# Optimization experiments

Measured on AMD Instinct MI355X. Metric: run time of the kernel, lower is better.

The kernel has to match this reference:

```python
import jax, jax.numpy as jnp
import numpy as np

D_MODEL = 2048
EXPAND = 2
D_INNER = EXPAND * D_MODEL          # 4096 == d_ssm
D_STATE = 128
NGROUPS = 1
HEADDIM = 64
NHEADS = D_INNER // HEADDIM          # 64
D_CONV = 4
CHUNK = 128
D_XBC = D_INNER + 2 * NGROUPS * D_STATE   # 4352
D_IN_PROJ = 2 * D_INNER + 2 * NGROUPS * D_STATE + NHEADS  # 8512
EPS = 1e-5


def setup_inputs() -> dict:
    key = jax.random.key(0)
    ks = jax.random.split(key, 9)
    u = jax.random.normal(ks[0], (2, 2048, D_MODEL), dtype=jnp.float32)
    W_in = jax.random.normal(ks[1], (D_IN_PROJ, D_MODEL), dtype=jnp.float32) / np.sqrt(D_MODEL)
    conv_w = jax.random.normal(ks[2], (D_XBC, D_CONV), dtype=jnp.float32) / np.sqrt(D_CONV)
    conv_b = jax.random.normal(ks[3], (D_XBC,), dtype=jnp.float32) * 0.1
    dt_bias = jnp.log(jnp.expm1(jax.random.uniform(ks[4], (NHEADS,), minval=0.001, maxval=0.1)))
    A_log = jnp.log(jax.random.uniform(ks[5], (NHEADS,), minval=1.0, maxval=16.0))
    D = jnp.ones((NHEADS,), dtype=jnp.float32)
    norm_weight = jnp.ones((D_INNER,), dtype=jnp.float32)
    W_out = jax.random.normal(ks[8], (D_MODEL, D_INNER), dtype=jnp.float32) / np.sqrt(D_INNER)
    return {"u": u, "W_in": W_in, "conv_w": conv_w, "conv_b": conv_b,
            "dt_bias": dt_bias, "A_log": A_log, "D": D,
            "norm_weight": norm_weight, "W_out": W_out}


def _causal_conv1d(xBC, conv_w, conv_b):
    # xBC: [b, l, d]; depthwise causal conv of width D_CONV, then SiLU
    x = jnp.transpose(xBC, (0, 2, 1))                      # [b, d, l]
    x = jnp.pad(x, ((0, 0), (0, 0), (D_CONV - 1, 0)))
    y = jax.lax.conv_general_dilated(
        x, conv_w[:, None, :], window_strides=(1,), padding='VALID',
        feature_group_count=D_XBC, dimension_numbers=('NCH', 'OIH', 'NCH'))
    y = y + conv_b[None, :, None]
    return jnp.transpose(jax.nn.silu(y), (0, 2, 1))        # [b, l, d]


def _ssd(x, dt, A, B, C, D):
    # x: [b,l,h,p]; dt: [b,l,h] (post-softplus); A: [h]; B,C: [b,l,g,n]; D: [h]
    b, L, h, p = x.shape
    n = B.shape[-1]
    c = L // CHUNK
    hpg = h // NGROUPS
    Bh = jnp.repeat(B, hpg, axis=2)                        # [b,l,h,n]
    Ch = jnp.repeat(C, hpg, axis=2)
    xr = x.reshape(b, c, CHUNK, h, p)
    dtr = dt.reshape(b, c, CHUNK, h)
    Br = Bh.reshape(b, c, CHUNK, h, n)
    Cr = Ch.reshape(b, c, CHUNK, h, n)
    xdt = xr * dtr[..., None]                              # [b,c,l,h,p]
    dA = jnp.transpose((dt * A[None, None, :]).reshape(b, c, CHUNK, h), (0, 3, 1, 2))  # [b,h,c,l]
    A_cs = jnp.cumsum(dA, axis=-1)                         # [b,h,c,l]
    # intra-chunk decay matrix L[i,j] = exp(sum_{j+1..i} dA), lower-triangular
    diff = A_cs[..., :, None] - A_cs[..., None, :]         # [b,h,c,l,s]
    mask = jnp.tril(jnp.ones((CHUNK, CHUNK), dtype=bool))
    Lmat = jnp.where(mask, jnp.exp(jnp.where(mask, diff, 0.0)), 0.0)
    Y_diag = jnp.einsum('bclhn,bcshn,bhcls,bcshp->bclhp', Cr, Br, Lmat, xdt)
    decay_states = jnp.exp(A_cs[..., -1:] - A_cs)          # [b,h,c,l]
    states = jnp.einsum('bclhn,bhcl,bclhp->bchpn', Br, decay_states, xdt)
    chunk_decay = jnp.exp(A_cs[..., -1])                   # [b,h,c]
    # inter-chunk recurrence over c chunks
    def step(carry, inp):
        s, d = inp                                         # s:[b,h,p,n], d:[b,h]
        return carry * d[..., None, None] + s, carry
    init = jnp.zeros((b, h, p, n), dtype=x.dtype)
    _, prev = jax.lax.scan(step, init,
                           (jnp.transpose(states, (1, 0, 2, 3, 4)),
                            jnp.transpose(chunk_decay, (2, 0, 1))))
    prev_states = jnp.transpose(prev, (1, 0, 2, 3, 4))     # [b,c,h,p,n]
    Y_off = jnp.einsum('bclhn,bchpn,bhcl->bclhp', Cr, prev_states, jnp.exp(A_cs))
    Y = (Y_diag + Y_off).reshape(b, L, h, p) + x * D[None, None, :, None]
    return Y


def reference(u, W_in, conv_w, conv_b, dt_bias, A_log, D, norm_weight, W_out):
    b, L, _ = u.shape
    zxbcdt = jnp.einsum('bld,ed->ble', u, W_in)            # [b,l,8512]
    z = zxbcdt[..., :D_INNER]
    xBC = zxbcdt[..., D_INNER:D_INNER + D_XBC]
    dt = zxbcdt[..., D_INNER + D_XBC:]                     # [b,l,h]
    xBC = _causal_conv1d(xBC, conv_w, conv_b)
    x = xBC[..., :D_INNER]
    B = xBC[..., D_INNER:D_INNER + NGROUPS * D_STATE].reshape(b, L, NGROUPS, D_STATE)
    C = xBC[..., D_INNER + NGROUPS * D_STATE:].reshape(b, L, NGROUPS, D_STATE)
    dt = jax.nn.softplus(dt + dt_bias[None, None, :])
    A = -jnp.exp(A_log)
    y = _ssd(x.reshape(b, L, NHEADS, HEADDIM), dt, A, B, C, D)
    y = y.reshape(b, L, D_INNER)
    # gated RMSNorm (norm_before_gate=False): norm(y * silu(z))
    yg = y * jax.nn.silu(z)
    y = yg * jax.lax.rsqrt(jnp.mean(yg * yg, axis=-1, keepdims=True) + EPS) * norm_weight
    return jnp.einsum('bld,ed->ble', y, W_out)
```

## Files before the change

kernel.cpp:

```cpp
#include <hip/hip_runtime.h>
#include <cstdint>
#include <cstddef>

#define SEQ     2048
#define NBATCH  2
#define BL      (NBATCH*SEQ)
#define DMODEL  2048
#define DINNER  4096
#define DSTATE  128
#define HEADDIM 64
#define NHEADS  64
#define DXBC    4352
#define DPROJ   8512
#define NPAD    8704
#define NCHUNK  16
#define CHUNKL  128

typedef __bf16 bf16x8_t __attribute__((ext_vector_type(8)));
typedef float f32x4_t __attribute__((ext_vector_type(4)));
typedef unsigned short u16x8_t __attribute__((ext_vector_type(8)));
typedef unsigned short u16x4_t __attribute__((ext_vector_type(4)));
typedef __attribute__((address_space(1))) unsigned int as1_u32;
typedef __attribute__((address_space(3))) unsigned int as3_u32;

__device__ __forceinline__ unsigned short f2bf(float f) {
  unsigned u = __builtin_bit_cast(unsigned, f);
  u += 0x7FFFu + ((u >> 16) & 1u);
  return (unsigned short)(u >> 16);
}
__device__ __forceinline__ float bf2f(unsigned short h) {
  unsigned u = ((unsigned)h) << 16;
  return __builtin_bit_cast(float, u);
}
__device__ __forceinline__ void gload16(const void* g, void* l) {
  __builtin_amdgcn_global_load_lds((const as1_u32*)g, (as3_u32*)l, 16, 0, 0);
}
__device__ __forceinline__ f32x4_t mfma16(u16x8_t a, u16x8_t b, f32x4_t c) {
  return __builtin_amdgcn_mfma_f32_16x16x32_bf16(
      __builtin_bit_cast(bf16x8_t, a), __builtin_bit_cast(bf16x8_t, b), c, 0, 0, 0);
}
__device__ __forceinline__ float siluf(float x) { return x / (1.f + __expf(-x)); }

#define GB_U   (BL * DMODEL / 4 / 256)
#define GB_WIN (NPAD * DMODEL / 4 / 256)
__global__ __launch_bounds__(256) void cvt_uw_kernel(const float* __restrict__ u,
                                                     unsigned short* __restrict__ u_bf,
                                                     const float* __restrict__ W_in,
                                                     unsigned short* __restrict__ win_bf) {
  int blk = blockIdx.x;
  if (blk < GB_U) {
    int idx = (blk * 256 + threadIdx.x) * 4;
    float4 v = *(const float4*)&u[idx];
    u16x4_t o; o[0] = f2bf(v.x); o[1] = f2bf(v.y); o[2] = f2bf(v.z); o[3] = f2bf(v.w);
    *(u16x4_t*)&u_bf[idx] = o;
  } else {
    int idx = ((blk - GB_U) * 256 + threadIdx.x) * 4;
    int e = idx / DMODEL;
    u16x4_t o;
    if (e < DPROJ) {
      float4 v = *(const float4*)&W_in[idx];
      o[0] = f2bf(v.x); o[1] = f2bf(v.y); o[2] = f2bf(v.z); o[3] = f2bf(v.w);
    } else {
      o[0] = 0; o[1] = 0; o[2] = 0; o[3] = 0;
    }
    *(u16x4_t*)&win_bf[idx] = o;
  }
}

template <int WM, bool BF16OUT>
__global__ __launch_bounds__(512, 2) void gemm256_kernel(const unsigned short* __restrict__ A,
                                                         const unsigned short* __restrict__ B,
                                                         void* __restrict__ Cp,
                                                         int M, int N, int K, int gx) {
  constexpr int BM  = 32 * WM;
  constexpr int AUB = BM * 64;
  constexpr int BUB = 16384;
  constexpr int BUF = AUB + BUB;
  constexpr int LA  = AUB / 8192;
  constexpr int LB  = 2;
  constexpr int LT  = LA + LB;
  __shared__ __attribute__((aligned(16))) char lds[4 * BUF];

  const int nwg = gridDim.x;
  const int q8 = nwg >> 3;
  const int lid = blockIdx.x;
  const int newid = (lid & 7) * q8 + (lid >> 3);
  const int band = newid / (gx * 4);
  const int idx  = newid % (gx * 4);
  const int n0 = (idx >> 2) * 256;
  const int m0 = (band * 4 + (idx & 3)) * BM;

  const int t = threadIdx.x, lane = t & 63, w = t >> 6;
  const int wm = w >> 2, wn = w & 3;
  const int NK = K >> 5;
  const int kslot = (lane >> 4) * 16;

  f32x4_t acc[WM][4];
#pragma unroll
  for (int i = 0; i < WM; ++i)
#pragma unroll
    for (int j = 0; j < 4; ++j) acc[i][j] = (f32x4_t){0.f, 0.f, 0.f, 0.f};

  auto stage_unit = [&](int u) {
    if (u >= 2 * NK) return;
    const int Tt = u >> 1;
    char* base = lds + (Tt & 3) * BUF + ((u & 1) ? AUB : 0);
    const unsigned short* G = (u & 1) ? B : A;
    const int g0 = (u & 1) ? n0 : m0;
    const int k0 = Tt << 5;
    if (u & 1) {
#pragma unroll
      for (int i = 0; i < LB; ++i) {
        int o = i * 8192 + t * 16;
        int row = o >> 6;
        int cb = (o & 63) ^ (((row >> 1) & 3) << 4);
        gload16(&G[(size_t)(g0 + row) * K + k0 + (cb >> 1)], base + o);
      }
    } else {
#pragma unroll
      for (int i = 0; i < LA; ++i) {
        int o = i * 8192 + t * 16;
        int row = o >> 6;
        int cb = (o & 63) ^ (((row >> 1) & 3) << 4);
        gload16(&G[(size_t)(g0 + row) * K + k0 + (cb >> 1)], base + o);
      }
    }
  };
  auto rdA = [&](int bq, int mr) -> u16x8_t {
    int row = wm * (BM / 2) + mr * 16 + (lane & 15);
    int byte = bq * BUF + row * 64 + (kslot ^ (((row >> 1) & 3) << 4));
    return *(const u16x8_t*)(lds + byte);
  };
  auto rdB = [&](int bq, int nr) -> u16x8_t {
    int row = wn * 64 + nr * 16 + (lane & 15);
    int byte = bq * BUF + AUB + row * 64 + (kslot ^ (((row >> 1) & 3) << 4));
    return *(const u16x8_t*)(lds + byte);
  };

#pragma unroll
  for (int u = 0; u < 6; ++u) stage_unit(u);

  for (int T = 0; T < NK; ++T) {
    const int bq = T & 3;
    if (T <= NK - 3)      { if constexpr (LT == 4) asm volatile("s_waitcnt vmcnt(8)" ::: "memory");
                            else                   asm volatile("s_waitcnt vmcnt(6)" ::: "memory"); }
    else if (T == NK - 2) { if constexpr (LT == 4) asm volatile("s_waitcnt vmcnt(4)" ::: "memory");
                            else                   asm volatile("s_waitcnt vmcnt(3)" ::: "memory"); }
    else                  asm volatile("s_waitcnt vmcnt(0)" ::: "memory");
    __builtin_amdgcn_s_barrier();
    asm volatile("" ::: "memory");
    __builtin_amdgcn_sched_barrier(0);

    u16x8_t af[WM], bfr[4];
#pragma unroll
    for (int mr = 0; mr < WM; ++mr) af[mr] = rdA(bq, mr);
    bfr[0] = rdB(bq, 0);
    bfr[1] = rdB(bq, 1);
    stage_unit(2 * T + 6);
    __builtin_amdgcn_s_setprio(1);
#pragma unroll
    for (int mr = 0; mr < WM; ++mr) {
      acc[mr][0] = mfma16(af[mr], bfr[0], acc[mr][0]);
      acc[mr][1] = mfma16(af[mr], bfr[1], acc[mr][1]);
    }
    __builtin_amdgcn_s_setprio(0);
    bfr[2] = rdB(bq, 2);
    bfr[3] = rdB(bq, 3);
    stage_unit(2 * T + 7);
    __builtin_amdgcn_s_setprio(1);
#pragma unroll
    for (int mr = 0; mr < WM; ++mr) {
      acc[mr][2] = mfma16(af[mr], bfr[2], acc[mr][2]);
      acc[mr][3] = mfma16(af[mr], bfr[3], acc[mr][3]);
    }
    __builtin_amdgcn_s_setprio(0);
  }

#pragma unroll
  for (int mr = 0; mr < WM; ++mr) {
    const int mbase = m0 + wm * (BM / 2) + mr * 16 + (lane >> 4) * 4;
#pragma unroll
    for (int nr = 0; nr < 4; ++nr) {
      const int n = n0 + wn * 64 + nr * 16 + (lane & 15);
#pragma unroll
      for (int r = 0; r < 4; ++r) {
        if (BF16OUT) ((unsigned short*)Cp)[(size_t)(mbase + r) * N + n] = f2bf(acc[mr][nr][r]);
        else         ((float*)Cp)[(size_t)(mbase + r) * N + n] = acc[mr][nr][r];
      }
    }
  }
}

#define GB_WOUT (DMODEL * DINNER / 4 / 256)
#define GB_CONV (BL * (DXBC / 8) / 256)
#define GB_DT   (NBATCH * NHEADS * NCHUNK / 2)
__global__ __launch_bounds__(256) void postg1_kernel(const float* __restrict__ W_out,
                                                     unsigned short* __restrict__ wout_bf,
                                                     const unsigned short* __restrict__ zx,
                                                     const float* __restrict__ conv_w,
                                                     const float* __restrict__ conv_b,
                                                     unsigned short* __restrict__ xc,
                                                     const float* __restrict__ dt_bias,
                                                     const float* __restrict__ A_log,
                                                     float* __restrict__ dt_soft,
                                                     float* __restrict__ Acs,
                                                     float* __restrict__ cdecay) {
  __shared__ float sbuf[256];
  int blk = blockIdx.x;
  int t = threadIdx.x;
  if (blk < GB_WOUT) {
    int idx = (blk * 256 + t) * 4;
    float4 v = *(const float4*)&W_out[idx];
    u16x4_t o; o[0] = f2bf(v.x); o[1] = f2bf(v.y); o[2] = f2bf(v.z); o[3] = f2bf(v.w);
    *(u16x4_t*)&wout_bf[idx] = o;
  } else if (blk < GB_WOUT + GB_CONV) {
    int idx = (blk - GB_WOUT) * 256 + t;
    int e8 = (idx % (DXBC / 8)) * 8;
    int bl = idx / (DXBC / 8);
    int l = bl % SEQ, b = bl / SEQ;
    float acc[8];
#pragma unroll
    for (int j = 0; j < 8; ++j) acc[j] = conv_b[e8 + j];
    const unsigned short* zrow = zx + (size_t)b * SEQ * NPAD + DINNER + e8;
#pragma unroll
    for (int wi = 0; wi < 4; ++wi) {
      int ll = l - 3 + wi;
      if (ll >= 0) {
        u16x8_t v = *(const u16x8_t*)(zrow + (size_t)ll * NPAD);
#pragma unroll
        for (int j = 0; j < 8; ++j) acc[j] += bf2f(v[j]) * conv_w[(e8 + j) * 4 + wi];
      }
    }
    u16x8_t o;
#pragma unroll
    for (int j = 0; j < 8; ++j) o[j] = f2bf(siluf(acc[j]));
    *(u16x8_t*)(xc + (size_t)bl * DXBC + e8) = o;
  } else {
    int id = (blk - GB_WOUT - GB_CONV) * 2 + (t >> 7);
    int i = t & 127;
    int c = id & 15, h = (id >> 4) & 63, b = id >> 10;
    int l = c * CHUNKL + i;
    float raw = bf2f(zx[((size_t)b * SEQ + l) * NPAD + (DINNER + DXBC) + h]) + dt_bias[h];
    float dt = (raw > 20.f) ? raw : log1pf(__expf(raw));
    dt_soft[((size_t)b * 64 + h) * SEQ + l] = dt;
    float A = -__expf(A_log[h]);
    float* sb = sbuf + (t >> 7) * 128;
    sb[i] = dt * A;
    __syncthreads();
    for (int ofs = 1; ofs < 128; ofs <<= 1) {
      float v = (i >= ofs) ? sb[i - ofs] : 0.f;
      __syncthreads();
      sb[i] += v;
      __syncthreads();
    }
    float cs = sb[i];
    Acs[(((size_t)b * 64 + h) * 16 + c) * 128 + i] = cs;
    if (i == 127) cdecay[((size_t)b * 64 + h) * 16 + c] = __expf(cs);
  }
}

#define GB_XDT (NBATCH * NHEADS * NCHUNK)
__global__ __launch_bounds__(256) void xdtbtr_kernel(const unsigned short* __restrict__ xc,
                                                     const float* __restrict__ dt_soft,
                                                     unsigned short* __restrict__ xdtT,
                                                     unsigned short* __restrict__ BT) {
  __shared__ __attribute__((aligned(16))) char smem[33536];
  int blk = blockIdx.x;
  int t = threadIdx.x;
  if (blk < GB_XDT) {
    int lt = blk & 15, h = (blk >> 4) & 63, b = blk >> 10;
    unsigned short (*tile)[66] = (unsigned short(*)[66])smem;
    float* dts = (float*)(smem + 16896);
    const unsigned short* xg = xc + ((size_t)b * SEQ + lt * 128) * DXBC + h * 64;
#pragma unroll
    for (int k = 0; k < 32; ++k) {
      int idx = t + k * 256;
      int row = idx >> 6, col = idx & 63;
      tile[row][col] = xg[(size_t)row * DXBC + col];
    }
    if (t < 128) dts[t] = dt_soft[((size_t)b * 64 + h) * SEQ + lt * 128 + t];
    __syncthreads();
    unsigned short* xo = xdtT + (((size_t)b * 64 + h) * 64) * SEQ + lt * 128;
#pragma unroll
    for (int k = 0; k < 32; ++k) {
      int idx = t + k * 256;
      int p = idx >> 7, j = idx & 127;
      xo[(size_t)p * SEQ + j] = f2bf(bf2f(tile[j][p]) * dts[j]);
    }
  } else {
    int bb = blk - GB_XDT;
    int lt = bb & 15, b = bb >> 4;
    unsigned short (*tile)[129] = (unsigned short(*)[129])smem;
    const unsigned short* src = xc + ((size_t)b * SEQ + lt * 128) * DXBC + DINNER;
#pragma unroll
    for (int k = 0; k < 64; ++k) {
      int idx = t + k * 256;
      int j = idx >> 7, n = idx & 127;
      tile[j][n] = src[(size_t)j * DXBC + n];
    }
    __syncthreads();
    unsigned short* dst = BT + (size_t)b * 128 * SEQ + lt * 128;
#pragma unroll
    for (int k = 0; k < 64; ++k) {
      int idx = t + k * 256;
      int n = idx >> 7, j = idx & 127;
      dst[(size_t)n * SEQ + j] = tile[j][n];
    }
  }
}

__global__ __launch_bounds__(256) void ssd_states_kernel(const unsigned short* __restrict__ BT,
                                                         const unsigned short* __restrict__ xdtT,
                                                         const float* __restrict__ Acs,
                                                         unsigned short* __restrict__ states) {
  int blk = blockIdx.x;
  int h = blk & 63, c = (blk >> 6) & 15, b = blk >> 10;
  __shared__ unsigned short BTs[128 * 128];
  __shared__ unsigned short xs[64 * 128];
  __shared__ float dec[128];
  int t = threadIdx.x, lane = t & 63, w = t >> 6, wr = w >> 1, wc = w & 1;
  int srow = t >> 4, scol = (t & 15) * 8;
  const unsigned short* BTb = BT + (size_t)b * 128 * SEQ + c * 128;
#pragma unroll
  for (int s = 0; s < 8; ++s) {
    int r = s * 16 + srow;
    gload16(&BTb[(size_t)r * SEQ + scol], &BTs[r * 128 + scol]);
  }
  const unsigned short* xb = xdtT + (((size_t)b * 64 + h) * 64) * SEQ + c * 128;
#pragma unroll
  for (int s = 0; s < 4; ++s) {
    int r = s * 16 + srow;
    gload16(&xb[(size_t)r * SEQ + scol], &xs[r * 128 + scol]);
  }
  const float* acsr = Acs + (((size_t)b * 64 + h) * 16 + c) * 128;
  float alast = acsr[127];
  if (t < 128) dec[t] = __expf(alast - acsr[t]);
  __syncthreads();

  f32x4_t acc[2][4];
#pragma unroll
  for (int i = 0; i < 2; ++i)
#pragma unroll
    for (int j = 0; j < 4; ++j) acc[i][j] = (f32x4_t){0.f, 0.f, 0.f, 0.f};
#pragma unroll
  for (int ks = 0; ks < 4; ++ks) {
    const int kk = ks * 32 + (lane >> 4) * 8;
    float d8[8];
#pragma unroll
    for (int e = 0; e < 8; ++e) d8[e] = dec[kk + e];
    u16x8_t af[2], bfr[4];
#pragma unroll
    for (int i = 0; i < 2; ++i) {
      u16x8_t raw = *(const u16x8_t*)&xs[(wr * 32 + i * 16 + (lane & 15)) * 128 + kk];
      u16x8_t sc;
#pragma unroll
      for (int e = 0; e < 8; ++e) sc[e] = f2bf(bf2f(raw[e]) * d8[e]);
      af[i] = sc;
    }
#pragma unroll
    for (int j = 0; j < 4; ++j)
      bfr[j] = *(const u16x8_t*)&BTs[(wc * 64 + j * 16 + (lane & 15)) * 128 + kk];
#pragma unroll
    for (int i = 0; i < 2; ++i)
#pragma unroll
      for (int j = 0; j < 4; ++j) acc[i][j] = mfma16(af[i], bfr[j], acc[i][j]);
  }
  unsigned short* so = states + ((((size_t)b * 16 + c) * 64 + h) * 64) * 128;
#pragma unroll
  for (int i = 0; i < 2; ++i) {
    int pbase = wr * 32 + i * 16 + (lane >> 4) * 4;
#pragma unroll
    for (int j = 0; j < 4; ++j) {
      int n = wc * 64 + j * 16 + (lane & 15);
#pragma unroll
      for (int r = 0; r < 4; ++r) so[(size_t)(pbase + r) * 128 + n] = f2bf(acc[i][j][r]);
    }
  }
}

__global__ __launch_bounds__(256) void ssd_scan_kernel(const unsigned short* __restrict__ states,
                                                       const float* __restrict__ cdecay,
                                                       unsigned short* __restrict__ prevb) {
  int blk = blockIdx.x;
  int s = blk & 7, h = (blk >> 3) & 63, b = blk >> 9;
  int t = threadIdx.x;
  const size_t eoff = (size_t)s * 1024 + t * 4;
  const float* cd = cdecay + ((size_t)b * 64 + h) * 16;
  u16x4_t vals[16];
#pragma unroll
  for (int c = 0; c < 16; ++c) {
    const unsigned short* sp = states + (((size_t)(b * 16 + c) * 64 + h) * 64) * 128 + eoff;
    vals[c] = *(const u16x4_t*)sp;
  }
  float carry[4] = {0.f, 0.f, 0.f, 0.f};
#pragma unroll
  for (int c = 0; c < 16; ++c) {
    unsigned short* pp = prevb + (((size_t)(b * 16 + c) * 64 + h) * 64) * 128 + eoff;
    u16x4_t o;
#pragma unroll
    for (int k = 0; k < 4; ++k) o[k] = f2bf(carry[k]);
    *(u16x4_t*)pp = o;
    float d = cd[c];
#pragma unroll
    for (int k = 0; k < 4; ++k) carry[k] = carry[k] * d + bf2f(vals[c][k]);
  }
}

__global__ __launch_bounds__(256) void ssd_y_kernel(const unsigned short* __restrict__ xc,
                                                    const unsigned short* __restrict__ xdtT,
                                                    const unsigned short* __restrict__ prevb,
                                                    const float* __restrict__ Acs,
                                                    const float* __restrict__ Dp,
                                                    unsigned short* __restrict__ Y) {
  int blk = blockIdx.x;
  int h = blk & 63, c = (blk >> 6) & 15, b = blk >> 10;
  __shared__ unsigned short Bs[128 * 128];
  __shared__ unsigned short Cs[128 * 128];
  __shared__ unsigned short xs[64 * 128];
  int t = threadIdx.x, lane = t & 63, w = t >> 6, wr = w >> 1, wc = w & 1;
  int srow = t >> 4, scol = (t & 15) * 8;
  const unsigned short* Bg = xc + ((size_t)b * SEQ + c * 128) * DXBC + DINNER;
  const unsigned short* Cg = Bg + DSTATE;
#pragma unroll
  for (int s = 0; s < 8; ++s) {
    int r = s * 16 + srow;
    gload16(&Bg[(size_t)r * DXBC + scol], &Bs[r * 128 + scol]);
    gload16(&Cg[(size_t)r * DXBC + scol], &Cs[r * 128 + scol]);
  }
  const unsigned short* xg = xdtT + (((size_t)b * 64 + h) * 64) * SEQ + c * 128;
#pragma unroll
  for (int s = 0; s < 4; ++s) {
    int r = s * 16 + srow;
    gload16(&xg[(size_t)r * SEQ + scol], &xs[r * 128 + scol]);
  }
  const unsigned short* pg = prevb + ((((size_t)b * 16 + c) * 64 + h) * 64) * 128;
  u16x8_t pf_all[4][2];
#pragma unroll
  for (int ks = 0; ks < 4; ++ks) {
    const int kk = ks * 32 + (lane >> 4) * 8;
#pragma unroll
    for (int j = 0; j < 2; ++j)
      pf_all[ks][j] = *(const u16x8_t*)&pg[(size_t)(wc * 32 + j * 16 + (lane & 15)) * 128 + kk];
  }
  const float* acsr = Acs + (((size_t)b * 64 + h) * 16 + c) * 128;
  __syncthreads();

  f32x4_t cbt[4][4];
#pragma unroll
  for (int i = 0; i < 4; ++i)
#pragma unroll
    for (int j = 0; j < 4; ++j) cbt[i][j] = (f32x4_t){0.f, 0.f, 0.f, 0.f};
#pragma unroll
  for (int ks = 0; ks < 4; ++ks) {
    const int kk = ks * 32 + (lane >> 4) * 8;
    u16x8_t af[4], bfr[4];
#pragma unroll
    for (int i = 0; i < 4; ++i) {
      af[i]  = *(const u16x8_t*)&Bs[(wr * 64 + i * 16 + (lane & 15)) * 128 + kk];
      bfr[i] = *(const u16x8_t*)&Cs[(wc * 64 + i * 16 + (lane & 15)) * 128 + kk];
    }
#pragma unroll
    for (int i = 0; i < 4; ++i)
#pragma unroll
      for (int j = 0; j < 4; ++j) cbt[i][j] = mfma16(af[i], bfr[j], cbt[i][j]);
  }
  __syncthreads();
#pragma unroll
  for (int fi = 0; fi < 4; ++fi) {
#pragma unroll
    for (int fj = 0; fj < 4; ++fj) {
      int i = wc * 64 + fj * 16 + (lane & 15);
      int jb = wr * 64 + fi * 16 + (lane >> 4) * 4;
      float ai = acsr[i];
      u16x4_t m4;
#pragma unroll
      for (int r = 0; r < 4; ++r) {
        int j = jb + r;
        float v = (i >= j) ? cbt[fi][fj][r] * __expf(ai - acsr[j]) : 0.f;
        m4[r] = f2bf(v);
      }
      *(u16x4_t*)&Bs[i * 128 + jb] = m4;
    }
  }
  __syncthreads();

  f32x4_t accY[4][2], accO[4][2];
#pragma unroll
  for (int i = 0; i < 4; ++i)
#pragma unroll
    for (int j = 0; j < 2; ++j) {
      accY[i][j] = (f32x4_t){0.f, 0.f, 0.f, 0.f};
      accO[i][j] = (f32x4_t){0.f, 0.f, 0.f, 0.f};
    }
#pragma unroll
  for (int ks = 0; ks < 4; ++ks) {
    const int kk = ks * 32 + (lane >> 4) * 8;
    u16x8_t af[4], bfr[2], cf[4];
#pragma unroll
    for (int i = 0; i < 4; ++i) {
      af[i] = *(const u16x8_t*)&Bs[(wr * 64 + i * 16 + (lane & 15)) * 128 + kk];
      cf[i] = *(const u16x8_t*)&Cs[(wr * 64 + i * 16 + (lane & 15)) * 128 + kk];
    }
#pragma unroll
    for (int j = 0; j < 2; ++j)
      bfr[j] = *(const u16x8_t*)&xs[(wc * 32 + j * 16 + (lane & 15)) * 128 + kk];
#pragma unroll
    for (int i = 0; i < 4; ++i)
#pragma unroll
      for (int j = 0; j < 2; ++j) {
        accY[i][j] = mfma16(af[i], bfr[j], accY[i][j]);
        accO[i][j] = mfma16(cf[i], pf_all[ks][j], accO[i][j]);
      }
  }
  float Dh = Dp[h];
  unsigned short* Yo = Y + ((size_t)b * SEQ + c * 128) * DINNER + h * 64;
  const unsigned short* xo = xc + ((size_t)b * SEQ + c * 128) * DXBC + h * 64;
#pragma unroll
  for (int fi = 0; fi < 4; ++fi) {
    int ibase = wr * 64 + fi * 16 + (lane >> 4) * 4;
#pragma unroll
    for (int r = 0; r < 4; ++r) {
      int i = ibase + r;
      float esc = __expf(acsr[i]);
#pragma unroll
      for (int fj = 0; fj < 2; ++fj) {
        int p = wc * 32 + fj * 16 + (lane & 15);
        float v = accY[fi][fj][r] + accO[fi][fj][r] * esc + bf2f(xo[(size_t)i * DXBC + p]) * Dh;
        Yo[(size_t)i * DINNER + p] = f2bf(v);
      }
    }
  }
}

__global__ __launch_bounds__(256) void norm_kernel(const unsigned short* __restrict__ Y,
                                                   const unsigned short* __restrict__ zx,
                                                   const float* __restrict__ nw,
                                                   unsigned short* __restrict__ yn) {
  int bl = blockIdx.x;
  const unsigned short* yr = Y + (size_t)bl * DINNER;
  const unsigned short* zr = zx + (size_t)bl * NPAD;
  int t = threadIdx.x;
  int base = t * 16;
  u16x8_t y0 = *(const u16x8_t*)&yr[base], y1 = *(const u16x8_t*)&yr[base + 8];
  u16x8_t z0 = *(const u16x8_t*)&zr[base], z1 = *(const u16x8_t*)&zr[base + 8];
  float vals[16];
  float ss = 0.f;
#pragma unroll
  for (int k = 0; k < 8; ++k) {
    float g = bf2f(y0[k]) * siluf(bf2f(z0[k]));
    vals[k] = g; ss += g * g;
  }
#pragma unroll
  for (int k = 0; k < 8; ++k) {
    float g = bf2f(y1[k]) * siluf(bf2f(z1[k]));
    vals[8 + k] = g; ss += g * g;
  }
#pragma unroll
  for (int o = 32; o > 0; o >>= 1) ss += __shfl_down(ss, o, 64);
  __shared__ float red[4];
  if ((t & 63) == 0) red[t >> 6] = ss;
  __syncthreads();
  float tot = red[0] + red[1] + red[2] + red[3];
  float rs = rsqrtf(tot * (1.f / (float)DINNER) + 1e-5f);
  u16x8_t o0, o1;
#pragma unroll
  for (int k = 0; k < 8; ++k) {
    o0[k] = f2bf(vals[k] * rs * nw[base + k]);
    o1[k] = f2bf(vals[8 + k] * rs * nw[base + 8 + k]);
  }
  *(u16x8_t*)&yn[(size_t)bl * DINNER + base] = o0;
  *(u16x8_t*)&yn[(size_t)bl * DINNER + base + 8] = o1;
}

extern "C" void kernel_launch(void* const* d_in, const int* in_sizes, int n_in,
                              void* d_out, int out_size, void* d_ws, size_t ws_size,
                              hipStream_t stream) {
  const float* u       = (const float*)d_in[0];
  const float* W_in    = (const float*)d_in[1];
  const float* conv_w  = (const float*)d_in[2];
  const float* conv_b  = (const float*)d_in[3];
  const float* dt_bias = (const float*)d_in[4];
  const float* A_log   = (const float*)d_in[5];
  const float* Dv      = (const float*)d_in[6];
  const float* norm_w  = (const float*)d_in[7];
  const float* W_out   = (const float*)d_in[8];
  float* out = (float*)d_out;
  (void)in_sizes; (void)n_in; (void)out_size;

  const size_t SZ_UBF    = (size_t)BL * DMODEL * 2;
  const size_t SZ_WIN    = (size_t)NPAD * DMODEL * 2;
  const size_t SZ_XDTT   = (size_t)NBATCH * NHEADS * HEADDIM * SEQ * 2;
  const size_t SZ_ZX     = (size_t)BL * NPAD * 2;
  const size_t SZ_XC     = (size_t)BL * DXBC * 2;
  const size_t SZ_BT     = (size_t)NBATCH * DSTATE * SEQ * 2;
  const size_t SZ_DTS    = (size_t)NBATCH * NHEADS * SEQ * 4;
  const size_t SZ_ACS    = (size_t)NBATCH * NHEADS * NCHUNK * 128 * 4;
  const size_t SZ_CDEC   = (size_t)NBATCH * NHEADS * NCHUNK * 4;
  const size_t SZ_STATES = (size_t)NBATCH * NCHUNK * NHEADS * HEADDIM * DSTATE * 2;
  const size_t SZ_PREV   = (size_t)NBATCH * NCHUNK * NHEADS * HEADDIM * DSTATE * 2;
  const size_t REGION_A  = SZ_UBF + SZ_WIN;

  char* ws = (char*)d_ws;
  size_t off = 0;
  auto alloc = [&](size_t bytes) { char* p = ws + off; off += (bytes + 255) & ~(size_t)255; return p; };

  char* regionA = alloc(REGION_A);
  unsigned short* zx     = (unsigned short*)alloc(SZ_ZX);
  unsigned short* xc     = (unsigned short*)alloc(SZ_XC);
  unsigned short* BT     = (unsigned short*)alloc(SZ_BT);
  float* dt_soft         = (float*)alloc(SZ_DTS);
  float* Acs             = (float*)alloc(SZ_ACS);
  float* cdecay          = (float*)alloc(SZ_CDEC);
  char* statesYb         = alloc(SZ_STATES);
  char* prevYn           = alloc(SZ_PREV);
  if (off > ws_size) return;

  unsigned short* u_bf    = (unsigned short*)regionA;
  unsigned short* win_bf  = (unsigned short*)(regionA + SZ_UBF);
  unsigned short* xdtT    = (unsigned short*)regionA;
  unsigned short* wout_bf = (unsigned short*)(regionA + SZ_XDTT);
  unsigned short* states  = (unsigned short*)statesYb;
  unsigned short* Yb      = (unsigned short*)statesYb;
  unsigned short* prevb   = (unsigned short*)prevYn;
  unsigned short* yn      = (unsigned short*)prevYn;

  cvt_uw_kernel<<<dim3(GB_U + GB_WIN), dim3(256), 0, stream>>>(u, u_bf, W_in, win_bf);

  gemm256_kernel<8, true><<<dim3((NPAD / 256) * (BL / 256)), dim3(512), 0, stream>>>(
      u_bf, win_bf, zx, BL, NPAD, DMODEL, NPAD / 256);

  postg1_kernel<<<dim3(GB_WOUT + GB_CONV + GB_DT), dim3(256), 0, stream>>>(
      W_out, wout_bf, zx, conv_w, conv_b, xc, dt_bias, A_log, dt_soft, Acs, cdecay);

  xdtbtr_kernel<<<dim3(GB_XDT + NBATCH * (SEQ / 128)), dim3(256), 0, stream>>>(
      xc, dt_soft, xdtT, BT);

  ssd_states_kernel<<<dim3(NBATCH * NCHUNK * NHEADS), dim3(256), 0, stream>>>(BT, xdtT, Acs, states);
  ssd_scan_kernel<<<dim3(NBATCH * NHEADS * 8), dim3(256), 0, stream>>>(states, cdecay, prevb);
  ssd_y_kernel<<<dim3(NBATCH * NCHUNK * NHEADS), dim3(256), 0, stream>>>(xc, xdtT, prevb, Acs, Dv, Yb);

  norm_kernel<<<dim3(BL), dim3(256), 0, stream>>>(Yb, zx, norm_w, yn);

  gemm256_kernel<4, false><<<dim3((DMODEL / 256) * (BL / 128)), dim3(512), 0, stream>>>(
      yn, wout_bf, out, BL, DMODEL, DINNER, DMODEL / 256);
}
```

Before: 545.2 us.

## Replace input-projection GEMM with 8-phase ping-pong pipelined 256x256 kernel

Adds a new GEMM kernel for the input projection with a 256x256 tile and 128KB of double-buffered LDS, which limits it to one block per CU. The K loop is split into eight phases that interleave half-tile global loads with MFMA work, using barriers, setprio and explicit vmcnt waits. It also remaps block IDs across 8 groups, presumably for XCD-aware L2 locality. The goal is to hide global-load latency better than the previous gemm256 kernel, at the cost of lower occupancy and more barriers.

```diff
diff --git a/kernel.cpp b/kernel.cpp
--- a/kernel.cpp
+++ b/kernel.cpp
@@ -64,6 +64,141 @@
       o[0] = 0; o[1] = 0; o[2] = 0; o[3] = 0;
     }
     *(u16x4_t*)&win_bf[idx] = o;
+  }
+}
+
+template <bool BF16OUT>
+__global__ __launch_bounds__(512, 1) void gemm8p_kernel(const unsigned short* __restrict__ A,
+                                                        const unsigned short* __restrict__ B,
+                                                        void* __restrict__ Cp,
+                                                        int M, int N, int K, int gx) {
+  __shared__ __attribute__((aligned(16))) char lds[131072];
+  const int nwg = gridDim.x;
+  const int q8 = nwg >> 3;
+  const int lid = blockIdx.x;
+  const int newid = (lid & 7) * q8 + (lid >> 3);
+  const int band = newid / (gx * 4);
+  const int idx  = newid % (gx * 4);
+  const int n0 = (idx >> 2) * 256;
+  const int m0 = (band * 4 + (idx & 3)) * 256;
+  const int t = threadIdx.x, lane = t & 63, w = t >> 6;
+  const int wm = w >> 2, wn = w & 3;
+  const int NK = K >> 6;
+  const int NT = NK >> 1;
+
+  f32x4_t acc[8][4];
+#pragma unroll
+  for (int i = 0; i < 8; ++i)
+#pragma unroll
+    for (int j = 0; j < 4; ++j) acc[i][j] = (f32x4_t){0.f, 0.f, 0.f, 0.f};
+
+  auto stage_half = [&](int tile, int half) {
+    if (tile >= NK) return;
+    const bool isB = half >= 2;
+    const int hh = half & 1;
+    const unsigned short* G = isB ? B : A;
+    const int g0 = (isB ? n0 : m0) + hh * 128;
+    const int k0 = tile << 6;
+    char* base = lds + (tile & 1) * 65536 + (isB ? 32768 : 0) + hh * 16384;
+#pragma unroll
+    for (int i = 0; i < 2; ++i) {
+      int o = i * 8192 + t * 16;
+      int row = o >> 7;
+      int sl  = (o >> 4) & 7;
+      gload16(&G[(size_t)(g0 + row) * K + k0 + ((sl ^ (row & 7)) << 3)], base + o);
+    }
+  };
+  auto rdA = [&](int buf, int mr, int kk) -> u16x8_t {
+    int row = wm * 128 + mr * 16 + (lane & 15);
+    int sl = kk * 4 + (lane >> 4);
+    int byte = buf * 65536 + row * 128 + (((sl ^ (row & 7))) << 4);
+    return *(const u16x8_t*)(lds + byte);
+  };
+  auto rdB = [&](int buf, int nr, int kk) -> u16x8_t {
+    int row = wn * 64 + nr * 16 + (lane & 15);
+    int sl = kk * 4 + (lane >> 4);
+    int byte = buf * 65536 + 32768 + row * 128 + (((sl ^ (row & 7))) << 4);
+    return *(const u16x8_t*)(lds + byte);
+  };
+
+  u16x8_t af[4][2], bf[4][2];
+
+#define PH_SYNC() do { __builtin_amdgcn_s_barrier(); \
+    asm volatile("s_waitcnt lgkmcnt(0)" ::: "memory"); \
+    __builtin_amdgcn_sched_barrier(0); } while (0)
+#define PH_END() __builtin_amdgcn_s_barrier()
+
+  auto mm = [&](int mrBase, int nrBase) {
+    __builtin_amdgcn_s_setprio(1);
+#pragma unroll
+    for (int m = 0; m < 4; ++m)
+#pragma unroll
+      for (int n = 0; n < 2; ++n) {
+        acc[mrBase + m][nrBase + n] = mfma16(af[m][0], bf[nrBase + n][0], acc[mrBase + m][nrBase + n]);
+        acc[mrBase + m][nrBase + n] = mfma16(af[m][1], bf[nrBase + n][1], acc[mrBase + m][nrBase + n]);
+      }
+    __builtin_amdgcn_s_setprio(0);
+  };
+
+  stage_half(0, 0); stage_half(0, 1); stage_half(0, 2); stage_half(0, 3);
+  stage_half(1, 2); stage_half(1, 3);
+  asm volatile("s_waitcnt vmcnt(4)" ::: "memory");
+  __builtin_amdgcn_s_barrier();
+
+  for (int j = 0; j < NT; ++j) {
+    const bool last = (j == NT - 1);
+    const int t1 = 2 * j + 1;
+#pragma unroll
+    for (int m = 0; m < 4; ++m) { af[m][0] = rdA(0, m, 0); af[m][1] = rdA(0, m, 1); }
+#pragma unroll
+    for (int n = 0; n < 2; ++n) { bf[n][0] = rdB(0, n, 0); bf[n][1] = rdB(0, n, 1); }
+    stage_half(t1, 0);
+    PH_SYNC(); mm(0, 0); PH_END();
+    bf[2][0] = rdB(0, 2, 0); bf[2][1] = rdB(0, 2, 1);
+    bf[3][0] = rdB(0, 3, 0); bf[3][1] = rdB(0, 3, 1);
+    stage_half(t1, 1);
+    PH_SYNC(); mm(0, 2); PH_END();
+#pragma unroll
+    for (int m = 0; m < 4; ++m) { af[m][0] = rdA(0, 4 + m, 0); af[m][1] = rdA(0, 4 + m, 1); }
+    stage_half(2 * j + 2, 2);
+    PH_SYNC(); mm(4, 0); PH_END();
+    stage_half(2 * j + 2, 3);
+    if (!last) asm volatile("s_waitcnt vmcnt(4)" ::: "memory");
+    else       asm volatile("s_waitcnt vmcnt(0)" ::: "memory");
+    PH_SYNC(); mm(4, 2); PH_END();
+#pragma unroll
+    for (int m = 0; m < 4; ++m) { af[m][0] = rdA(1, m, 0); af[m][1] = rdA(1, m, 1); }
+#pragma unroll
+    for (int n = 0; n < 2; ++n) { bf[n][0] = rdB(1, n, 0); bf[n][1] = rdB(1, n, 1); }
+    stage_half(2 * j + 2, 0);
+    PH_SYNC(); mm(0, 0); PH_END();
+    bf[2][0] = rdB(1, 2, 0); bf[2][1] = rdB(1, 2, 1);
+    bf[3][0] = rdB(1, 3, 0); bf[3][1] = rdB(1, 3, 1);
+    stage_half(2 * j + 2, 1);
+    PH_SYNC(); mm(0, 2); PH_END();
+#pragma unroll
+    for (int m = 0; m < 4; ++m) { af[m][0] = rdA(1, 4 + m, 0); af[m][1] = rdA(1, 4 + m, 1); }
+    stage_half(2 * j + 3, 2);
+    PH_SYNC(); mm(4, 0); PH_END();
+    stage_half(2 * j + 3, 3);
+    if (!last) asm volatile("s_waitcnt vmcnt(4)" ::: "memory");
+    PH_SYNC(); mm(4, 2); PH_END();
+  }
+#undef PH_SYNC
+#undef PH_END
+
+#pragma unroll
+  for (int mr = 0; mr < 8; ++mr) {
+    const int mbase = m0 + wm * 128 + mr * 16 + (lane >> 4) * 4;
+#pragma unroll
+    for (int nr = 0; nr < 4; ++nr) {
+      const int n = n0 + wn * 64 + nr * 16 + (lane & 15);
+#pragma unroll
+      for (int r = 0; r < 4; ++r) {
+        if (BF16OUT) ((unsigned short*)Cp)[(size_t)(mbase + r) * N + n] = f2bf(acc[mr][nr][r]);
+        else         ((float*)Cp)[(size_t)(mbase + r) * N + n] = acc[mr][nr][r];
+      }
+    }
   }
 }
 
@@ -626,7 +761,7 @@
 
   cvt_uw_kernel<<<dim3(GB_U + GB_WIN), dim3(256), 0, stream>>>(u, u_bf, W_in, win_bf);
 
-  gemm256_kernel<8, true><<<dim3((NPAD / 256) * (BL / 256)), dim3(512), 0, stream>>>(
+  gemm8p_kernel<true><<<dim3((NPAD / 256) * (BL / 256)), dim3(512), 0, stream>>>(
       u_bf, win_bf, zx, BL, NPAD, DMODEL, NPAD / 256);
 
   postg1_kernel<<<dim3(GB_WOUT + GB_CONV + GB_DT), dim3(256), 0, stream>>>(
```

After: 554.1 us. No clear change (+1.6%).

## Precompute per-chunk C·Bᵀ once and share it across heads in ssd_y

Applied to the files above, without the earlier changes.

With NGROUPS=1 every head of a chunk multiplies the same B and C, so the C·Bᵀ product was recomputed 64 times per chunk. Extra blocks in the transpose kernel now compute this 128x128 product once per (batch, chunk) and store it in fp32 global memory. ssd_y_kernel reads it back instead of loading B into LDS and running the MFMA loop, which drops the B load and one barrier. The cost is 4 MB of extra workspace and fp32 global reads per block; only 32 blocks do the shared product, reading B and C directly from global memory without LDS staging.

```diff
diff --git a/kernel.cpp b/kernel.cpp
--- a/kernel.cpp
+++ b/kernel.cpp
@@ -260,10 +260,12 @@
 }
 
 #define GB_XDT (NBATCH * NHEADS * NCHUNK)
+#define GB_BTR (NBATCH * (SEQ / 128))
 __global__ __launch_bounds__(256) void xdtbtr_kernel(const unsigned short* __restrict__ xc,
                                                      const float* __restrict__ dt_soft,
                                                      unsigned short* __restrict__ xdtT,
-                                                     unsigned short* __restrict__ BT) {
+                                                     unsigned short* __restrict__ BT,
+                                                     float* __restrict__ cbtG) {
   __shared__ __attribute__((aligned(16))) char smem[33536];
   int blk = blockIdx.x;
   int t = threadIdx.x;
@@ -287,7 +289,7 @@
       int p = idx >> 7, j = idx & 127;
       xo[(size_t)p * SEQ + j] = f2bf(bf2f(tile[j][p]) * dts[j]);
     }
-  } else {
+  } else if (blk < GB_XDT + GB_BTR) {
     int bb = blk - GB_XDT;
     int lt = bb & 15, b = bb >> 4;
     unsigned short (*tile)[129] = (unsigned short(*)[129])smem;
@@ -305,6 +307,42 @@
       int idx = t + k * 256;
       int n = idx >> 7, j = idx & 127;
       dst[(size_t)n * SEQ + j] = tile[j][n];
+    }
+  } else {
+    int id = blk - GB_XDT - GB_BTR;
+    int c = id & 15, b = id >> 4;
+    int lane = t & 63, w4 = t >> 6;
+    int wr = w4 >> 1, wc = w4 & 1;
+    const unsigned short* Bg = xc + ((size_t)b * SEQ + c * 128) * DXBC + DINNER;
+    const unsigned short* Cg = Bg + DSTATE;
+    f32x4_t cbt[4][4];
+#pragma unroll
+    for (int i = 0; i < 4; ++i)
+#pragma unroll
+      for (int j = 0; j < 4; ++j) cbt[i][j] = (f32x4_t){0.f, 0.f, 0.f, 0.f};
+#pragma unroll
+    for (int ks = 0; ks < 4; ++ks) {
+      const int kk = ks * 32 + (lane >> 4) * 8;
+      u16x8_t af[4], bfr[4];
+#pragma unroll
+      for (int i = 0; i < 4; ++i) {
+        af[i]  = *(const u16x8_t*)&Bg[(size_t)(wr * 64 + i * 16 + (lane & 15)) * DXBC + kk];
+        bfr[i] = *(const u16x8_t*)&Cg[(size_t)(wc * 64 + i * 16 + (lane & 15)) * DXBC + kk];
+      }
+#pragma unroll
+      for (int i = 0; i < 4; ++i)
+#pragma unroll
+        for (int j = 0; j < 4; ++j) cbt[i][j] = mfma16(af[i], bfr[j], cbt[i][j]);
+    }
+    float* dst = cbtG + ((size_t)(b * 16 + c) * 128) * 128;
+#pragma unroll
+    for (int fi = 0; fi < 4; ++fi) {
+#pragma unroll
+      for (int fj = 0; fj < 4; ++fj) {
+        int i = wc * 64 + fj * 16 + (lane & 15);
+        int jb = wr * 64 + fi * 16 + (lane >> 4) * 4;
+        *(f32x4_t*)&dst[(size_t)i * 128 + jb] = cbt[fi][fj];
+      }
     }
   }
 }
@@ -410,21 +448,20 @@
                                                     const unsigned short* __restrict__ xdtT,
                                                     const unsigned short* __restrict__ prevb,
                                                     const float* __restrict__ Acs,
+                                                    const float* __restrict__ cbtG,
                                                     const float* __restrict__ Dp,
                                                     unsigned short* __restrict__ Y) {
   int blk = blockIdx.x;
   int h = blk & 63, c = (blk >> 6) & 15, b = blk >> 10;
-  __shared__ unsigned short Bs[128 * 128];
+  __shared__ unsigned short Ms[128 * 128];
   __shared__ unsigned short Cs[128 * 128];
   __shared__ unsigned short xs[64 * 128];
   int t = threadIdx.x, lane = t & 63, w = t >> 6, wr = w >> 1, wc = w & 1;
   int srow = t >> 4, scol = (t & 15) * 8;
-  const unsigned short* Bg = xc + ((size_t)b * SEQ + c * 128) * DXBC + DINNER;
-  const unsigned short* Cg = Bg + DSTATE;
+  const unsigned short* Cg = xc + ((size_t)b * SEQ + c * 128) * DXBC + DINNER + DSTATE;
 #pragma unroll
   for (int s = 0; s < 8; ++s) {
     int r = s * 16 + srow;
-    gload16(&Bg[(size_t)r * DXBC + scol], &Bs[r * 128 + scol]);
     gload16(&Cg[(size_t)r * DXBC + scol], &Cs[r * 128 + scol]);
   }
   const unsigned short* xg = xdtT + (((size_t)b * 64 + h) * 64) * SEQ + c * 128;
@@ -443,43 +480,23 @@
       pf_all[ks][j] = *(const u16x8_t*)&pg[(size_t)(wc * 32 + j * 16 + (lane & 15)) * 128 + kk];
   }
   const float* acsr = Acs + (((size_t)b * 64 + h) * 16 + c) * 128;
-  __syncthreads();
-
-  f32x4_t cbt[4][4];
-#pragma unroll
-  for (int i = 0; i < 4; ++i)
-#pragma unroll
-    for (int j = 0; j < 4; ++j) cbt[i][j] = (f32x4_t){0.f, 0.f, 0.f, 0.f};
-#pragma unroll
-  for (int ks = 0; ks < 4; ++ks) {
-    const int kk = ks * 32 + (lane >> 4) * 8;
-    u16x8_t af[4], bfr[4];
-#pragma unroll
-    for (int i = 0; i < 4; ++i) {
-      af[i]  = *(const u16x8_t*)&Bs[(wr * 64 + i * 16 + (lane & 15)) * 128 + kk];
-      bfr[i] = *(const u16x8_t*)&Cs[(wc * 64 + i * 16 + (lane & 15)) * 128 + kk];
-    }
-#pragma unroll
-    for (int i = 0; i < 4; ++i)
-#pragma unroll
-      for (int j = 0; j < 4; ++j) cbt[i][j] = mfma16(af[i], bfr[j], cbt[i][j]);
-  }
-  __syncthreads();
+  const float* cbtB = cbtG + ((size_t)(b * 16 + c) * 128) * 128;
 #pragma unroll
   for (int fi = 0; fi < 4; ++fi) {
 #pragma unroll
     for (int fj = 0; fj < 4; ++fj) {
       int i = wc * 64 + fj * 16 + (lane & 15);
       int jb = wr * 64 + fi * 16 + (lane >> 4) * 4;
+      f32x4_t cb4 = *(const f32x4_t*)&cbtB[(size_t)i * 128 + jb];
       float ai = acsr[i];
       u16x4_t m4;
 #pragma unroll
       for (int r = 0; r < 4; ++r) {
         int j = jb + r;
-        float v = (i >= j) ? cbt[fi][fj][r] * __expf(ai - acsr[j]) : 0.f;
+        float v = (i >= j) ? cb4[r] * __expf(ai - acsr[j]) : 0.f;
         m4[r] = f2bf(v);
       }
-      *(u16x4_t*)&Bs[i * 128 + jb] = m4;
+      *(u16x4_t*)&Ms[i * 128 + jb] = m4;
     }
   }
   __syncthreads();
@@ -498,7 +515,7 @@
     u16x8_t af[4], bfr[2], cf[4];
 #pragma unroll
     for (int i = 0; i < 4; ++i) {
-      af[i] = *(const u16x8_t*)&Bs[(wr * 64 + i * 16 + (lane & 15)) * 128 + kk];
+      af[i] = *(const u16x8_t*)&Ms[(wr * 64 + i * 16 + (lane & 15)) * 128 + kk];
       cf[i] = *(const u16x8_t*)&Cs[(wr * 64 + i * 16 + (lane & 15)) * 128 + kk];
     }
 #pragma unroll
@@ -596,6 +613,7 @@
   const size_t SZ_DTS    = (size_t)NBATCH * NHEADS * SEQ * 4;
   const size_t SZ_ACS    = (size_t)NBATCH * NHEADS * NCHUNK * 128 * 4;
   const size_t SZ_CDEC   = (size_t)NBATCH * NHEADS * NCHUNK * 4;
+  const size_t SZ_CBT    = (size_t)NBATCH * NCHUNK * 128 * 128 * 4;
   const size_t SZ_STATES = (size_t)NBATCH * NCHUNK * NHEADS * HEADDIM * DSTATE * 2;
   const size_t SZ_PREV   = (size_t)NBATCH * NCHUNK * NHEADS * HEADDIM * DSTATE * 2;
   const size_t REGION_A  = SZ_UBF + SZ_WIN;
@@ -611,6 +629,7 @@
   float* dt_soft         = (float*)alloc(SZ_DTS);
   float* Acs             = (float*)alloc(SZ_ACS);
   float* cdecay          = (float*)alloc(SZ_CDEC);
+  float* cbtG            = (float*)alloc(SZ_CBT);
   char* statesYb         = alloc(SZ_STATES);
   char* prevYn           = alloc(SZ_PREV);
   if (off > ws_size) return;
@@ -632,12 +651,13 @@
   postg1_kernel<<<dim3(GB_WOUT + GB_CONV + GB_DT), dim3(256), 0, stream>>>(
       W_out, wout_bf, zx, conv_w, conv_b, xc, dt_bias, A_log, dt_soft, Acs, cdecay);
 
-  xdtbtr_kernel<<<dim3(GB_XDT + NBATCH * (SEQ / 128)), dim3(256), 0, stream>>>(
-      xc, dt_soft, xdtT, BT);
+  xdtbtr_kernel<<<dim3(GB_XDT + GB_BTR + NBATCH * NCHUNK), dim3(256), 0, stream>>>(
+      xc, dt_soft, xdtT, BT, cbtG);
 
   ssd_states_kernel<<<dim3(NBATCH * NCHUNK * NHEADS), dim3(256), 0, stream>>>(BT, xdtT, Acs, states);
   ssd_scan_kernel<<<dim3(NBATCH * NHEADS * 8), dim3(256), 0, stream>>>(states, cdecay, prevb);
-  ssd_y_kernel<<<dim3(NBATCH * NCHUNK * NHEADS), dim3(256), 0, stream>>>(xc, xdtT, prevb, Acs, Dv, Yb);
+  ssd_y_kernel<<<dim3(NBATCH * NCHUNK * NHEADS), dim3(256), 0, stream>>>(
+      xc, xdtT, prevb, Acs, cbtG, Dv, Yb);
 
   norm_kernel<<<dim3(BL), dim3(256), 0, stream>>>(Yb, zx, norm_w, yn);
 
```

New measurement: 546.1 us, median of 2. Within noise of the previous version (+0.2%).
